# Kernel tuning notes

Hardware: AMD Instinct MI355X
Metric: run time of the kernel (lower is better)

Reference implementation:

```python
import jax, jax.numpy as jnp
import numpy as np

O, NI, F, D, NN, M = 2048, 16, 4, 128, 8, 8  # outfits, item slots, factors, dim, neighbors, valid slots
D2 = D // 2

def lrelu(x):
    return jax.nn.leaky_relu(x, 0.01)

def mlp2(x, W1, b1, W2, b2):
    # Linear -> LeakyReLU -> Linear -> LeakyReLU (Dropout is identity at inference)
    return lrelu(lrelu(x @ W1 + b1) @ W2 + b2)

def setup_inputs():
    ks = jax.random.split(jax.random.key(0), 16)
    s = 0.05
    pos = jnp.arange(NI)[None, :]
    outfit_items = jnp.where(pos < M, jax.random.randint(ks[0], (O, NI), 0, NI), -1)
    items_neighbor = jax.random.randint(ks[1], (O, NI, NN), -1, NI)
    items_feature = jax.random.normal(ks[2], (O, NI, D), dtype=jnp.float32)
    items_factors = jnp.zeros((O, NI, F, D), dtype=jnp.float32)
    p = {
        'cf_W1': jax.random.normal(ks[3], (F, D, D2)) * s,
        'cf_b1': jnp.zeros((F, D2)),
        'cf_W2': jax.random.normal(ks[4], (F, D2, D)) * s,
        'cf_b2': jnp.zeros((F, D)),
        'f2f_W1': jax.random.normal(ks[5], (D, D)) * s, 'f2f_b1': jnp.zeros((D,)),
        'f2f_W2': jax.random.normal(ks[6], (D, D)) * s, 'f2f_b2': jnp.zeros((D,)),
        'f2i_W1': jax.random.normal(ks[7], (D, D)) * s, 'f2i_b1': jnp.zeros((D,)),
        'f2i_W2': jax.random.normal(ks[8], (D, D)) * s, 'f2i_b2': jnp.zeros((D,)),
        'i2i_W1': jax.random.normal(ks[9], (D, D)) * s, 'i2i_b1': jnp.zeros((D,)),
        'i2i_W2': jax.random.normal(ks[10], (D, D)) * s, 'i2i_b2': jnp.zeros((D,)),
        'o2s_W': jax.random.normal(ks[11], (D, 1)) * s, 'o2s_b': jnp.zeros((1,)),
    }
    return dict(outfit_items=outfit_items, items_feature=items_feature,
                items_neighbor=items_neighbor, items_factors=items_factors, **p)

def _forward(outfit_items, items_feature, items_neighbor, items_factors,
             cf_W1, cf_b1, cf_W2, cf_b2, f2f_W1, f2f_b1, f2f_W2, f2f_b2,
             f2i_W1, f2i_b1, f2i_W2, f2i_b2, i2i_W1, i2i_b1, i2i_W2, i2i_b2,
             o2s_W, o2s_b):
    del items_factors  # creat_factors overwrites every entry in the original
    # --- creat_factors: per-factor 2-layer MLP on every item feature -> [O,NI,F,D]
    h = lrelu(jnp.einsum('oid,fde->oife', items_feature, cf_W1) + cf_b1)
    fac = lrelu(jnp.einsum('oife,fed->oifd', h, cf_W2) + cf_b2)

    # --- inter_factors: sequential over outfit slots; later slots read updated factors
    def outfit_fac(fac_o, oi_o, nbr_o):
        def step(f, i):
            valid = i != -1
            ic = jnp.maximum(i, 0)
            cand = jnp.concatenate([oi_o, nbr_o[ic]])                # [NI+NN]
            cm = (cand != -1) & (cand != i) & valid
            t = f[ic]                                                # [F,D] snapshot
            msg = mlp2(t[None] * f[jnp.maximum(cand, 0)],
                       f2f_W1, f2f_b1, f2f_W2, f2f_b2)               # [NI+NN,F,D]
            add = jnp.sum(jnp.where(cm[:, None, None], msg, 0.0), axis=0)
            return f.at[ic].add(jnp.where(valid, add, 0.0)), None
        f, _ = jax.lax.scan(step, fac_o, oi_o)
        return f
    fac = jax.vmap(outfit_fac)(fac, outfit_items, items_neighbor)

    # --- infer_items: feature[i] += sum_j f2i(fac[i,j]) for outfit members
    g = mlp2(fac, f2i_W1, f2i_b1, f2i_W2, f2i_b2).sum(axis=2)        # [O,NI,D]
    ic = jnp.maximum(outfit_items, 0)
    w = (outfit_items != -1).astype(g.dtype)                          # [O,NI]
    gsel = jnp.take_along_axis(g, ic[..., None], axis=1)
    scat = jax.vmap(lambda gs, idx, ww: jnp.zeros((NI, D), gs.dtype).at[idx].add(ww[:, None] * gs))
    feat = items_feature + scat(gsel, ic, w)

    # --- inter_items: sequential; current value detached (.data in original)
    def outfit_feat(fo_init, oi_o):
        jc = jnp.maximum(oi_o, 0)
        def step(fo, i):
            valid = i != -1
            ic_ = jnp.maximum(i, 0)
            t = jax.lax.stop_gradient(fo[ic_])
            msgs = mlp2(fo[jc], i2i_W1, i2i_b1, i2i_W2, i2i_b2)      # [NI,D]
            m = ((oi_o != -1) & (oi_o != i)).astype(fo.dtype)
            new = t + jnp.sum(m[:, None] * msgs, axis=0)
            return jnp.where(valid, fo.at[ic_].set(new), fo), None
        fo, _ = jax.lax.scan(step, fo_init, oi_o)
        return fo
    feat = jax.vmap(outfit_feat)(feat, outfit_items)

    # --- infer_outfit + score
    fsel = jnp.take_along_axis(feat, ic[..., None], axis=1)
    outfits = jnp.sum(w[..., None] * fsel, axis=1)                    # [O,D]
    scores = jax.nn.sigmoid(outfits @ o2s_W + o2s_b)[:, 0]            # [O]

    # --- com_loss: ||F F^T - I||_F^2 over valid slots (positional mask), / n_outfits
    G = jnp.einsum('oifd,oigd->oifg', fac, fac) - jnp.eye(F, dtype=fac.dtype)
    com = jnp.sum(w * jnp.sum(G * G, axis=(-1, -2))) / O
    return scores, jnp.reshape(com, (1,))

def reference(outfit_items, items_feature, items_neighbor, items_factors,
              cf_W1, cf_b1, cf_W2, cf_b2, f2f_W1, f2f_b1, f2f_W2, f2f_b2,
              f2i_W1, f2i_b1, f2i_W2, f2i_b2, i2i_W1, i2i_b1, i2i_W2, i2i_b2,
              o2s_W, o2s_b):
    return _forward(outfit_items, items_feature, items_neighbor, items_factors,
                    cf_W1, cf_b1, cf_W2, cf_b2, f2f_W1, f2f_b1, f2f_W2, f2f_b2,
                    f2i_W1, f2i_b1, f2i_W2, f2i_b2, i2i_W1, i2i_b1, i2i_W2, i2i_b2,
                    o2s_W, o2s_b)
```

## Files before the change

### kernel.cpp

```cpp
#include <hip/hip_runtime.h>
#include <hip/hip_bf16.h>
#include <math.h>


typedef __attribute__((ext_vector_type(8))) short short8;
typedef __attribute__((ext_vector_type(4))) float f32x4;

#define MFMA16(a, b, c) __builtin_amdgcn_mfma_f32_16x16x32_bf16(a, b, c, 0, 0, 0)

__device__ __forceinline__ float lrelu(float x) { return x > 0.0f ? x : 0.01f * x; }

__device__ __forceinline__ ushort f2bf(float f) {
  unsigned u = __builtin_bit_cast(unsigned, f);
  u += 0x7fffu + ((u >> 16) & 1u);
  return (ushort)(u >> 16);
}

__device__ __forceinline__ unsigned pk2(float a, float b) {
  float2 t; t.x = a; t.y = b;
  __hip_bfloat162 h = __float22bfloat162_rn(t);
  unsigned u;
  __builtin_memcpy(&u, &h, 4);
  return u;
}

__device__ __forceinline__ short8 load_bfrag(const float* __restrict__ W, int ldn,
                                             int kbase, int col) {
  short8 r;
#pragma unroll
  for (int j = 0; j < 8; ++j) r[j] = (short)f2bf(W[(kbase + j) * ldn + col]);
  return r;
}

__global__ void zero_com(float* out) { if (threadIdx.x == 0) out[2048] = 0.0f; }

__global__ __launch_bounds__(512, 4) void mfgn_kernel(
    const int* __restrict__ outfit_items,
    const float* __restrict__ items_feature,
    const int* __restrict__ items_neighbor,
    const float* __restrict__ cfW1, const float* __restrict__ cfb1,
    const float* __restrict__ cfW2, const float* __restrict__ cfb2,
    const float* __restrict__ f2fW1, const float* __restrict__ f2fb1,
    const float* __restrict__ f2fW2, const float* __restrict__ f2fb2,
    const float* __restrict__ f2iW1, const float* __restrict__ f2ib1,
    const float* __restrict__ f2iW2, const float* __restrict__ f2ib2,
    const float* __restrict__ i2iW1, const float* __restrict__ i2ib1,
    const float* __restrict__ i2iW2, const float* __restrict__ i2ib2,
    const float* __restrict__ o2sW, const float* __restrict__ o2sb,
    float* __restrict__ out)
{
  __shared__ float facL[16 * 528];
  __shared__ float featL[16 * 132];
  __shared__ ushort Xa[64 * 136] __attribute__((aligned(16)));
  __shared__ ushort hidB[64 * 136] __attribute__((aligned(16)));
  __shared__ float redE[8];
  __shared__ int oiL[16];
  __shared__ int nbrL[128];
  __shared__ int clAll[16 * 16];
  __shared__ int ncAll[16];
  __shared__ int vslL[16];
  __shared__ int refcntL[16];
  __shared__ int nvsL;

  const int o = blockIdx.x;
  const int tid = (int)threadIdx.x;
  const int lane = tid & 63;
  const int wid = tid >> 6;
  const int n16 = lane & 15;
  const int q = lane >> 4;
  const int kb = q * 8;
  const int col = wid * 16 + n16;

  if (tid < 16) oiL[tid] = outfit_items[o * 16 + tid];
  if (tid < 128) nbrL[tid] = items_neighbor[o * 128 + tid];
  {
    const int n = tid >> 5, d0 = (tid & 31) * 4;
    float4 v = *(const float4*)(items_feature + o * 2048 + tid * 4);
    *(float4*)(featL + n * 132 + d0) = v;
    uint2 pk; pk.x = pk2(v.x, v.y); pk.y = pk2(v.z, v.w);
    *(uint2*)(Xa + n * 136 + d0) = pk;
  }
  if (tid == 0) {
    int cnt = 0;
    for (int s = 0; s < 16; ++s) refcntL[s] = 0;
    for (int s = 0; s < 16; ++s) {
      int v = oiL[s];
      if (v != -1) { vslL[cnt++] = s; refcntL[v]++; }
    }
    nvsL = cnt;
  }
  for (int s = wid; s < 16; s += 8) {
    const int iv = outfit_items[o * 16 + s];
    if (iv == -1) { if (lane == 0) ncAll[s] = 0; continue; }
    int cand = -1;
    if (lane < 24) cand = (lane < 16) ? outfit_items[o * 16 + lane]
                                      : items_neighbor[o * 128 + iv * 8 + (lane - 16)];
    bool ok = (lane < 24) && (cand != -1) && (cand != iv);
    unsigned long long bm = __ballot(ok);
    if (ok) clAll[s * 16 + __popcll(bm & ((1ull << lane) - 1ull))] = cand;
    if (lane == 0) ncAll[s] = (int)__popcll(bm);
  }
  __syncthreads();
  const int nvs = nvsL;

  {
    const int f = wid & 3, half = wid >> 2;
    short8 wA[2][4];
#pragma unroll
    for (int etl = 0; etl < 2; ++etl)
#pragma unroll
      for (int kt = 0; kt < 4; ++kt)
        wA[etl][kt] = load_bfrag(cfW1 + f * 8192, 64, kt * 32 + kb, (half * 2 + etl) * 16 + n16);
    f32x4 acc[2];
    acc[0] = (f32x4){0.f,0.f,0.f,0.f}; acc[1] = (f32x4){0.f,0.f,0.f,0.f};
    for (int kt = 0; kt < 4; ++kt) {
      short8 x = *(const short8*)(Xa + n16 * 136 + kt * 32 + kb);
      acc[0] = MFMA16(wA[0][kt], x, acc[0]);
      acc[1] = MFMA16(wA[1][kt], x, acc[1]);
    }
#pragma unroll
    for (int etl = 0; etl < 2; ++etl) {
      f32x4 b1q = *(const f32x4*)(cfb1 + f * 64 + (half * 2 + etl) * 16 + q * 4);
      float h0 = lrelu(acc[etl][0] + b1q[0]), h1 = lrelu(acc[etl][1] + b1q[1]);
      float h2 = lrelu(acc[etl][2] + b1q[2]), h3 = lrelu(acc[etl][3] + b1q[3]);
      uint2 pk; pk.x = pk2(h0, h1); pk.y = pk2(h2, h3);
      *(uint2*)(hidB + (f * 16 + n16) * 136 + (half * 2 + etl) * 16 + q * 4) = pk;
    }
    __syncthreads();
    short8 wB[4][2];
#pragma unroll
    for (int ctl = 0; ctl < 4; ++ctl)
#pragma unroll
      for (int kt = 0; kt < 2; ++kt)
        wB[ctl][kt] = load_bfrag(cfW2 + f * 8192, 128, kt * 32 + kb, half * 64 + ctl * 16 + n16);
    f32x4 acc2[4];
#pragma unroll
    for (int ctl = 0; ctl < 4; ++ctl) acc2[ctl] = (f32x4){0.f,0.f,0.f,0.f};
    for (int kt = 0; kt < 2; ++kt) {
      short8 h = *(const short8*)(hidB + (f * 16 + n16) * 136 + kt * 32 + kb);
#pragma unroll
      for (int ctl = 0; ctl < 4; ++ctl) acc2[ctl] = MFMA16(h, wB[ctl][kt], acc2[ctl]);
    }
#pragma unroll
    for (int ctl = 0; ctl < 4; ++ctl) {
      int c = half * 64 + ctl * 16 + n16;
      float b2 = cfb2[f * 128 + c];
#pragma unroll
      for (int r = 0; r < 4; ++r)
        facL[(q * 4 + r) * 528 + f * 132 + c] = lrelu(acc2[ctl][r] + b2);
    }
    __syncthreads();
  }

  {
    short8 w1f[4], w2f[4];
#pragma unroll
    for (int kt = 0; kt < 4; ++kt) {
      w1f[kt] = load_bfrag(f2fW1, 128, kt * 32 + kb, col);
      w2f[kt] = load_bfrag(f2fW2, 128, kt * 32 + kb, col);
    }
    const f32x4 b1q = *(const f32x4*)(f2fb1 + wid * 16 + q * 4);
    const float b2v = f2fb2[col];
    const int rS = tid >> 3, kcS = tid & 7;
    const int fS = rS & 3, ciS = rS >> 2;
    const int k0 = kcS * 16;

    for (int s = 0; s < 16; ++s) {
      const int iv = oiL[s];
      if (iv == -1) continue;
      const int nc = ncAll[s];
      if (ciS < nc) {
        const int cit = clAll[s * 16 + ciS];
        const float* tp = facL + iv * 528 + fS * 132;
        const float* cp = facL + cit * 528 + fS * 132;
#pragma unroll
        for (int i2 = 0; i2 < 2; ++i2) {
          const int k = k0 + i2 * 8;
          float4 a0 = *(const float4*)(tp + k), a1 = *(const float4*)(tp + k + 4);
          float4 c0 = *(const float4*)(cp + k), c1 = *(const float4*)(cp + k + 4);
          uint4 u;
          u.x = pk2(a0.x * c0.x, a0.y * c0.y); u.y = pk2(a0.z * c0.z, a0.w * c0.w);
          u.z = pk2(a1.x * c1.x, a1.y * c1.y); u.w = pk2(a1.z * c1.z, a1.w * c1.w);
          *(uint4*)(Xa + rS * 136 + k) = u;
        }
      } else {
        uint4 z; z.x = z.y = z.z = z.w = 0;
        *(uint4*)(Xa + rS * 136 + k0) = z;
        *(uint4*)(Xa + rS * 136 + k0 + 8) = z;
      }
      __syncthreads();
      f32x4 acc[4];
#pragma unroll
      for (int mt = 0; mt < 4; ++mt) acc[mt] = (f32x4){0.f,0.f,0.f,0.f};
      for (int kt = 0; kt < 4; ++kt)
#pragma unroll
        for (int mt = 0; mt < 4; ++mt) {
          short8 x = *(const short8*)(Xa + (mt * 16 + n16) * 136 + kt * 32 + kb);
          acc[mt] = MFMA16(w1f[kt], x, acc[mt]);
        }
      __syncthreads();
#pragma unroll
      for (int mt = 0; mt < 4; ++mt) {
        float h0 = lrelu(acc[mt][0] + b1q[0]), h1 = lrelu(acc[mt][1] + b1q[1]);
        float h2 = lrelu(acc[mt][2] + b1q[2]), h3 = lrelu(acc[mt][3] + b1q[3]);
        uint2 pk; pk.x = pk2(h0, h1); pk.y = pk2(h2, h3);
        *(uint2*)(hidB + (mt * 16 + n16) * 136 + wid * 16 + q * 4) = pk;
      }
      __syncthreads();
      f32x4 acc2[4];
#pragma unroll
      for (int mt = 0; mt < 4; ++mt) acc2[mt] = (f32x4){0.f,0.f,0.f,0.f};
      for (int kt = 0; kt < 4; ++kt)
#pragma unroll
        for (int mt = 0; mt < 4; ++mt) {
          short8 h = *(const short8*)(hidB + (mt * 16 + n16) * 136 + kt * 32 + kb);
          acc2[mt] = MFMA16(h, w2f[kt], acc2[mt]);
        }
      float part[4] = {0.f, 0.f, 0.f, 0.f};
#pragma unroll
      for (int mt = 0; mt < 4; ++mt) {
        bool act = (mt * 4 + q) < nc;
        if (act)
#pragma unroll
          for (int r = 0; r < 4; ++r) part[r] += lrelu(acc2[mt][r] + b2v);
      }
#pragma unroll
      for (int r = 0; r < 4; ++r) {
        float v = part[r];
        v += __shfl_xor(v, 16);
        v += __shfl_xor(v, 32);
        part[r] = v;
      }
      if (q == 0) {
#pragma unroll
        for (int r = 0; r < 4; ++r)
          facL[iv * 528 + r * 132 + col] += part[r];
      }
      __syncthreads();
    }
  }

  {
    short8 w1f[4], w2f[4];
#pragma unroll
    for (int kt = 0; kt < 4; ++kt) {
      w1f[kt] = load_bfrag(f2iW1, 128, kt * 32 + kb, col);
      w2f[kt] = load_bfrag(f2iW2, 128, kt * 32 + kb, col);
    }
    const f32x4 b1q = *(const f32x4*)(f2ib1 + wid * 16 + q * 4);
    const float b2v = f2ib2[col];
    {
      const int r = tid >> 3, kc = tid & 7, k0 = kc * 16;
      const int f = r & 3, item = r >> 2;
      const float* sp = facL + item * 528 + f * 132;
#pragma unroll
      for (int i2 = 0; i2 < 2; ++i2) {
        const int k = k0 + i2 * 8;
        float4 a0 = *(const float4*)(sp + k), a1 = *(const float4*)(sp + k + 4);
        uint4 u;
        u.x = pk2(a0.x, a0.y); u.y = pk2(a0.z, a0.w);
        u.z = pk2(a1.x, a1.y); u.w = pk2(a1.z, a1.w);
        *(uint4*)(Xa + r * 136 + k) = u;
      }
    }
    __syncthreads();
    f32x4 acc[4];
#pragma unroll
    for (int mt = 0; mt < 4; ++mt) acc[mt] = (f32x4){0.f,0.f,0.f,0.f};
    for (int kt = 0; kt < 4; ++kt)
#pragma unroll
      for (int mt = 0; mt < 4; ++mt) {
        short8 x = *(const short8*)(Xa + (mt * 16 + n16) * 136 + kt * 32 + kb);
        acc[mt] = MFMA16(w1f[kt], x, acc[mt]);
      }
    __syncthreads();
#pragma unroll
    for (int mt = 0; mt < 4; ++mt) {
      float h0 = lrelu(acc[mt][0] + b1q[0]), h1 = lrelu(acc[mt][1] + b1q[1]);
      float h2 = lrelu(acc[mt][2] + b1q[2]), h3 = lrelu(acc[mt][3] + b1q[3]);
      uint2 pk; pk.x = pk2(h0, h1); pk.y = pk2(h2, h3);
      *(uint2*)(hidB + (mt * 16 + n16) * 136 + wid * 16 + q * 4) = pk;
    }
    __syncthreads();
    f32x4 acc2[4];
#pragma unroll
    for (int mt = 0; mt < 4; ++mt) acc2[mt] = (f32x4){0.f,0.f,0.f,0.f};
    for (int kt = 0; kt < 4; ++kt)
#pragma unroll
      for (int mt = 0; mt < 4; ++mt) {
        short8 h = *(const short8*)(hidB + (mt * 16 + n16) * 136 + kt * 32 + kb);
        acc2[mt] = MFMA16(h, w2f[kt], acc2[mt]);
      }
#pragma unroll
    for (int mt = 0; mt < 4; ++mt) {
      int item = mt * 4 + q;
      float g = 0.f;
#pragma unroll
      for (int r = 0; r < 4; ++r) g += lrelu(acc2[mt][r] + b2v);
      featL[item * 132 + col] += (float)refcntL[item] * g;
    }
    __syncthreads();
  }

  {
    short8 w1f[4], w2f[4];
#pragma unroll
    for (int kt = 0; kt < 4; ++kt) {
      w1f[kt] = load_bfrag(i2iW1, 128, kt * 32 + kb, col);
      w2f[kt] = load_bfrag(i2iW2, 128, kt * 32 + kb, col);
    }
    const f32x4 b1q = *(const f32x4*)(i2ib1 + wid * 16 + q * 4);
    const float b2v = i2ib2[col];
    const int rS = tid >> 3, kcS = tid & 7, k0 = kcS * 16;

    for (int u = 0; u < nvs; ++u) {
      const int iv = oiL[vslL[u]];
      if (rS < nvs) {
        const int it = oiL[vslL[rS]];
        const float* sp = featL + it * 132;
#pragma unroll
        for (int i2 = 0; i2 < 2; ++i2) {
          const int k = k0 + i2 * 8;
          float4 a0 = *(const float4*)(sp + k), a1 = *(const float4*)(sp + k + 4);
          uint4 uu;
          uu.x = pk2(a0.x, a0.y); uu.y = pk2(a0.z, a0.w);
          uu.z = pk2(a1.x, a1.y); uu.w = pk2(a1.z, a1.w);
          *(uint4*)(Xa + rS * 136 + k) = uu;
        }
      }
      __syncthreads();
      f32x4 acc;
      acc = (f32x4){0.f,0.f,0.f,0.f};
      for (int kt = 0; kt < 4; ++kt) {
        short8 x = *(const short8*)(Xa + n16 * 136 + kt * 32 + kb);
        acc = MFMA16(w1f[kt], x, acc);
      }
      __syncthreads();
      {
        float h0 = lrelu(acc[0] + b1q[0]), h1 = lrelu(acc[1] + b1q[1]);
        float h2 = lrelu(acc[2] + b1q[2]), h3 = lrelu(acc[3] + b1q[3]);
        uint2 pk; pk.x = pk2(h0, h1); pk.y = pk2(h2, h3);
        *(uint2*)(hidB + n16 * 136 + wid * 16 + q * 4) = pk;
      }
      __syncthreads();
      f32x4 acc2;
      acc2 = (f32x4){0.f,0.f,0.f,0.f};
      for (int kt = 0; kt < 4; ++kt) {
        short8 h = *(const short8*)(hidB + n16 * 136 + kt * 32 + kb);
        acc2 = MFMA16(h, w2f[kt], acc2);
      }
      float part = 0.f;
      if (q < 2) {
#pragma unroll
        for (int r = 0; r < 4; ++r) {
          int j = q * 4 + r;
          bool m = (j < nvs) && (oiL[vslL[j]] != iv);
          if (m) part += lrelu(acc2[r] + b2v);
        }
      }
      part += __shfl_xor(part, 16);
      if (q == 0) featL[iv * 132 + col] += part;
      __syncthreads();
    }
  }

  if (tid < 128) {
    float sum = 0.0f;
    for (int u = 0; u < nvs; ++u) sum += featL[oiL[vslL[u]] * 132 + tid];
    float v = sum * o2sW[tid];
#pragma unroll
    for (int off = 1; off < 64; off <<= 1) v += __shfl_xor(v, off);
    if (lane == 0) redE[wid] = v;
  }
  __syncthreads();
  if (tid == 0) {
    float t = redE[0] + redE[1] + o2sb[0];
    out[o] = 1.0f / (1.0f + expf(-t));
  }

  {
    const int n = tid >> 5, f = (tid >> 3) & 3, g = (tid >> 1) & 3, h = tid & 1;
    const float* pa = facL + n * 528 + f * 132 + h * 64;
    const float* pb = facL + n * 528 + g * 132 + h * 64;
    float dot = 0.0f;
    for (int i = 0; i < 16; ++i) {
      float4 a = *(const float4*)(pa + i * 4);
      float4 b = *(const float4*)(pb + i * 4);
      dot += a.x * b.x + a.y * b.y + a.z * b.z + a.w * b.w;
    }
    dot += __shfl_xor(dot, 1);
    float v = dot - ((f == g) ? 1.0f : 0.0f);
    float sq = (h == 0 && oiL[n] != -1) ? v * v : 0.0f;
#pragma unroll
    for (int off = 1; off < 64; off <<= 1) sq += __shfl_xor(sq, off);
    __syncthreads();
    if (lane == 0) redE[wid] = sq;
    __syncthreads();
    if (tid == 0) {
      float tot = 0.f;
#pragma unroll
      for (int w = 0; w < 8; ++w) tot += redE[w];
      atomicAdd(out + 2048, tot * (1.0f / 2048.0f));
    }
  }
}

extern "C" void kernel_launch(void* const* d_in, const int* in_sizes, int n_in,
                              void* d_out, int out_size, void* d_ws, size_t ws_size,
                              hipStream_t stream) {
  float* out = (float*)d_out;
  hipLaunchKernelGGL(zero_com, dim3(1), dim3(64), 0, stream, out);
  hipLaunchKernelGGL(mfgn_kernel, dim3(2048), dim3(512), 0, stream,
                     (const int*)d_in[0],
                     (const float*)d_in[1],
                     (const int*)d_in[2],
                     (const float*)d_in[4], (const float*)d_in[5],
                     (const float*)d_in[6], (const float*)d_in[7],
                     (const float*)d_in[8], (const float*)d_in[9],
                     (const float*)d_in[10], (const float*)d_in[11],
                     (const float*)d_in[12], (const float*)d_in[13],
                     (const float*)d_in[14], (const float*)d_in[15],
                     (const float*)d_in[16], (const float*)d_in[17],
                     (const float*)d_in[18], (const float*)d_in[19],
                     (const float*)d_in[20], (const float*)d_in[21],
                     out);
}
```

Before: 363.6 us.

## Store factors and features in bf16 shared memory and skip empty MFMA tiles

Factor and feature buffers in LDS change from fp32 to bf16 and are fed straight to the MFMAs, which removes the per-stage repacking copies and their barriers. An fp32 copy of each factor is kept in registers for exact accumulation, and the Gram matrix for the orthogonality loss is computed from those registers with shuffle reductions and shared atomics. The f2f MFMA loops skip row tiles beyond the candidate count. The smaller LDS footprint allows raising launch bounds to six blocks per CU. In exchange, the stored activations lose precision because feature accumulation goes through bf16 round-trips, and the i2i stage now weights neighbors by reference count over all rows.

Measured after the change: 988.9 us. 2.72x slower.

```diff
diff --git a/kernel.cpp b/kernel.cpp
--- a/kernel.cpp
+++ b/kernel.cpp
@@ -15,7 +15,12 @@
   u += 0x7fffu + ((u >> 16) & 1u);
   return (ushort)(u >> 16);
 }
-
+__device__ __forceinline__ float bflo(unsigned u) {
+  return __builtin_bit_cast(float, u << 16);
+}
+__device__ __forceinline__ float bfhi(unsigned u) {
+  return __builtin_bit_cast(float, u & 0xffff0000u);
+}
 __device__ __forceinline__ unsigned pk2(float a, float b) {
   float2 t; t.x = a; t.y = b;
   __hip_bfloat162 h = __float22bfloat162_rn(t);
@@ -23,7 +28,6 @@
   __builtin_memcpy(&u, &h, 4);
   return u;
 }
-
 __device__ __forceinline__ short8 load_bfrag(const float* __restrict__ W, int ldn,
                                              int kbase, int col) {
   short8 r;
@@ -34,7 +38,7 @@
 
 __global__ void zero_com(float* out) { if (threadIdx.x == 0) out[2048] = 0.0f; }
 
-__global__ __launch_bounds__(512, 4) void mfgn_kernel(
+__global__ __launch_bounds__(512, 6) void mfgn_kernel(
     const int* __restrict__ outfit_items,
     const float* __restrict__ items_feature,
     const int* __restrict__ items_neighbor,
@@ -49,14 +53,13 @@
     const float* __restrict__ o2sW, const float* __restrict__ o2sb,
     float* __restrict__ out)
 {
-  __shared__ float facL[16 * 528];
-  __shared__ float featL[16 * 132];
-  __shared__ ushort Xa[64 * 136] __attribute__((aligned(16)));
-  __shared__ ushort hidB[64 * 136] __attribute__((aligned(16)));
+  __shared__ ushort facB[64 * 136] __attribute__((aligned(16)));
+  __shared__ ushort featB[16 * 136] __attribute__((aligned(16)));
+  __shared__ ushort stg[64 * 136] __attribute__((aligned(16)));
+  __shared__ float comG[256];
   __shared__ float redE[8];
   __shared__ int oiL[16];
-  __shared__ int nbrL[128];
-  __shared__ int clAll[16 * 16];
+  __shared__ int clAll[256];
   __shared__ int ncAll[16];
   __shared__ int vslL[16];
   __shared__ int refcntL[16];
@@ -72,13 +75,12 @@
   const int col = wid * 16 + n16;
 
   if (tid < 16) oiL[tid] = outfit_items[o * 16 + tid];
-  if (tid < 128) nbrL[tid] = items_neighbor[o * 128 + tid];
+  if (tid < 256) comG[tid] = 0.0f;
   {
     const int n = tid >> 5, d0 = (tid & 31) * 4;
     float4 v = *(const float4*)(items_feature + o * 2048 + tid * 4);
-    *(float4*)(featL + n * 132 + d0) = v;
     uint2 pk; pk.x = pk2(v.x, v.y); pk.y = pk2(v.z, v.w);
-    *(uint2*)(Xa + n * 136 + d0) = pk;
+    *(uint2*)(featB + n * 136 + d0) = pk;
   }
   if (tid == 0) {
     int cnt = 0;
@@ -114,7 +116,7 @@
     f32x4 acc[2];
     acc[0] = (f32x4){0.f,0.f,0.f,0.f}; acc[1] = (f32x4){0.f,0.f,0.f,0.f};
     for (int kt = 0; kt < 4; ++kt) {
-      short8 x = *(const short8*)(Xa + n16 * 136 + kt * 32 + kb);
+      short8 x = *(const short8*)(featB + n16 * 136 + kt * 32 + kb);
       acc[0] = MFMA16(wA[0][kt], x, acc[0]);
       acc[1] = MFMA16(wA[1][kt], x, acc[1]);
     }
@@ -124,7 +126,7 @@
       float h0 = lrelu(acc[etl][0] + b1q[0]), h1 = lrelu(acc[etl][1] + b1q[1]);
       float h2 = lrelu(acc[etl][2] + b1q[2]), h3 = lrelu(acc[etl][3] + b1q[3]);
       uint2 pk; pk.x = pk2(h0, h1); pk.y = pk2(h2, h3);
-      *(uint2*)(hidB + (f * 16 + n16) * 136 + (half * 2 + etl) * 16 + q * 4) = pk;
+      *(uint2*)(stg + (f * 16 + n16) * 136 + (half * 2 + etl) * 16 + q * 4) = pk;
     }
     __syncthreads();
     short8 wB[4][2];
@@ -137,7 +139,7 @@
 #pragma unroll
     for (int ctl = 0; ctl < 4; ++ctl) acc2[ctl] = (f32x4){0.f,0.f,0.f,0.f};
     for (int kt = 0; kt < 2; ++kt) {
-      short8 h = *(const short8*)(hidB + (f * 16 + n16) * 136 + kt * 32 + kb);
+      short8 h = *(const short8*)(stg + (f * 16 + n16) * 136 + kt * 32 + kb);
 #pragma unroll
       for (int ctl = 0; ctl < 4; ++ctl) acc2[ctl] = MFMA16(h, wB[ctl][kt], acc2[ctl]);
     }
@@ -147,7 +149,7 @@
       float b2 = cfb2[f * 128 + c];
 #pragma unroll
       for (int r = 0; r < 4; ++r)
-        facL[(q * 4 + r) * 528 + f * 132 + c] = lrelu(acc2[ctl][r] + b2);
+        facB[((q * 4 + r) * 4 + f) * 136 + c] = f2bf(lrelu(acc2[ctl][r] + b2));
     }
     __syncthreads();
   }
@@ -161,32 +163,43 @@
     }
     const f32x4 b1q = *(const f32x4*)(f2fb1 + wid * 16 + q * 4);
     const float b2v = f2fb2[col];
+    float fac32[16];
+#pragma unroll
+    for (int rr = 0; rr < 4; ++rr)
+#pragma unroll
+      for (int f = 0; f < 4; ++f)
+        fac32[rr * 4 + f] = bflo((unsigned)facB[((q * 4 + rr) * 4 + f) * 136 + col]);
+
     const int rS = tid >> 3, kcS = tid & 7;
     const int fS = rS & 3, ciS = rS >> 2;
-    const int k0 = kcS * 16;
+    const int kcol = kcS * 16;
 
     for (int s = 0; s < 16; ++s) {
       const int iv = oiL[s];
       if (iv == -1) continue;
       const int nc = ncAll[s];
+      const int mtn = (nc + 3) >> 2;
       if (ciS < nc) {
         const int cit = clAll[s * 16 + ciS];
-        const float* tp = facL + iv * 528 + fS * 132;
-        const float* cp = facL + cit * 528 + fS * 132;
-#pragma unroll
-        for (int i2 = 0; i2 < 2; ++i2) {
-          const int k = k0 + i2 * 8;
-          float4 a0 = *(const float4*)(tp + k), a1 = *(const float4*)(tp + k + 4);
-          float4 c0 = *(const float4*)(cp + k), c1 = *(const float4*)(cp + k + 4);
-          uint4 u;
-          u.x = pk2(a0.x * c0.x, a0.y * c0.y); u.y = pk2(a0.z * c0.z, a0.w * c0.w);
-          u.z = pk2(a1.x * c1.x, a1.y * c1.y); u.w = pk2(a1.z * c1.z, a1.w * c1.w);
-          *(uint4*)(Xa + rS * 136 + k) = u;
-        }
+        const ushort* tp = facB + (iv * 4 + fS) * 136 + kcol;
+        const ushort* cp = facB + (cit * 4 + fS) * 136 + kcol;
+        uint4 ta = *(const uint4*)tp, tb = *(const uint4*)(tp + 8);
+        uint4 ca = *(const uint4*)cp, cb = *(const uint4*)(cp + 8);
+        uint4 u0, u1;
+        u0.x = pk2(bflo(ta.x) * bflo(ca.x), bfhi(ta.x) * bfhi(ca.x));
+        u0.y = pk2(bflo(ta.y) * bflo(ca.y), bfhi(ta.y) * bfhi(ca.y));
+        u0.z = pk2(bflo(ta.z) * bflo(ca.z), bfhi(ta.z) * bfhi(ca.z));
+        u0.w = pk2(bflo(ta.w) * bflo(ca.w), bfhi(ta.w) * bfhi(ca.w));
+        u1.x = pk2(bflo(tb.x) * bflo(cb.x), bfhi(tb.x) * bfhi(cb.x));
+        u1.y = pk2(bflo(tb.y) * bflo(cb.y), bfhi(tb.y) * bfhi(cb.y));
+        u1.z = pk2(bflo(tb.z) * bflo(cb.z), bfhi(tb.z) * bfhi(cb.z));
+        u1.w = pk2(bflo(tb.w) * bflo(cb.w), bfhi(tb.w) * bfhi(cb.w));
+        *(uint4*)(stg + rS * 136 + kcol) = u0;
+        *(uint4*)(stg + rS * 136 + kcol + 8) = u1;
       } else {
         uint4 z; z.x = z.y = z.z = z.w = 0;
-        *(uint4*)(Xa + rS * 136 + k0) = z;
-        *(uint4*)(Xa + rS * 136 + k0 + 8) = z;
+        *(uint4*)(stg + rS * 136 + kcol) = z;
+        *(uint4*)(stg + rS * 136 + kcol + 8) = z;
       }
       __syncthreads();
       f32x4 acc[4];
@@ -194,28 +207,31 @@
       for (int mt = 0; mt < 4; ++mt) acc[mt] = (f32x4){0.f,0.f,0.f,0.f};
       for (int kt = 0; kt < 4; ++kt)
 #pragma unroll
-        for (int mt = 0; mt < 4; ++mt) {
-          short8 x = *(const short8*)(Xa + (mt * 16 + n16) * 136 + kt * 32 + kb);
-          acc[mt] = MFMA16(w1f[kt], x, acc[mt]);
+        for (int mt = 0; mt < 4; ++mt)
+          if (mt < mtn) {
+            short8 x = *(const short8*)(stg + (mt * 16 + n16) * 136 + kt * 32 + kb);
+            acc[mt] = MFMA16(w1f[kt], x, acc[mt]);
+          }
+      __syncthreads();
+#pragma unroll
+      for (int mt = 0; mt < 4; ++mt)
+        if (mt < mtn) {
+          float h0 = lrelu(acc[mt][0] + b1q[0]), h1 = lrelu(acc[mt][1] + b1q[1]);
+          float h2 = lrelu(acc[mt][2] + b1q[2]), h3 = lrelu(acc[mt][3] + b1q[3]);
+          uint2 pk; pk.x = pk2(h0, h1); pk.y = pk2(h2, h3);
+          *(uint2*)(stg + (mt * 16 + n16) * 136 + wid * 16 + q * 4) = pk;
         }
-      __syncthreads();
-#pragma unroll
-      for (int mt = 0; mt < 4; ++mt) {
-        float h0 = lrelu(acc[mt][0] + b1q[0]), h1 = lrelu(acc[mt][1] + b1q[1]);
-        float h2 = lrelu(acc[mt][2] + b1q[2]), h3 = lrelu(acc[mt][3] + b1q[3]);
-        uint2 pk; pk.x = pk2(h0, h1); pk.y = pk2(h2, h3);
-        *(uint2*)(hidB + (mt * 16 + n16) * 136 + wid * 16 + q * 4) = pk;
-      }
       __syncthreads();
       f32x4 acc2[4];
 #pragma unroll
       for (int mt = 0; mt < 4; ++mt) acc2[mt] = (f32x4){0.f,0.f,0.f,0.f};
       for (int kt = 0; kt < 4; ++kt)
 #pragma unroll
-        for (int mt = 0; mt < 4; ++mt) {
-          short8 h = *(const short8*)(hidB + (mt * 16 + n16) * 136 + kt * 32 + kb);
-          acc2[mt] = MFMA16(h, w2f[kt], acc2[mt]);
-        }
+        for (int mt = 0; mt < 4; ++mt)
+          if (mt < mtn) {
+            short8 h = *(const short8*)(stg + (mt * 16 + n16) * 136 + kt * 32 + kb);
+            acc2[mt] = MFMA16(h, w2f[kt], acc2[mt]);
+          }
       float part[4] = {0.f, 0.f, 0.f, 0.f};
 #pragma unroll
       for (int mt = 0; mt < 4; ++mt) {
@@ -231,13 +247,30 @@
         v += __shfl_xor(v, 32);
         part[r] = v;
       }
-      if (q == 0) {
-#pragma unroll
-        for (int r = 0; r < 4; ++r)
-          facL[iv * 528 + r * 132 + col] += part[r];
-      }
-      __syncthreads();
-    }
+      if (q == (iv >> 2)) {
+        const int rr = iv & 3;
+#pragma unroll
+        for (int f = 0; f < 4; ++f) {
+          fac32[rr * 4 + f] += part[f];
+          facB[(iv * 4 + f) * 136 + col] = f2bf(fac32[rr * 4 + f]);
+        }
+      }
+      __syncthreads();
+    }
+
+#pragma unroll
+    for (int rr = 0; rr < 4; ++rr)
+#pragma unroll
+      for (int f = 0; f < 4; ++f)
+#pragma unroll
+        for (int g = 0; g < 4; ++g) {
+          float p = fac32[rr * 4 + f] * fac32[rr * 4 + g];
+          p += __shfl_xor(p, 1);
+          p += __shfl_xor(p, 2);
+          p += __shfl_xor(p, 4);
+          p += __shfl_xor(p, 8);
+          if (n16 == 0) atomicAdd(&comG[(q * 4 + rr) * 16 + f * 4 + g], p);
+        }
   }
 
   {
@@ -249,37 +282,21 @@
     }
     const f32x4 b1q = *(const f32x4*)(f2ib1 + wid * 16 + q * 4);
     const float b2v = f2ib2[col];
-    {
-      const int r = tid >> 3, kc = tid & 7, k0 = kc * 16;
-      const int f = r & 3, item = r >> 2;
-      const float* sp = facL + item * 528 + f * 132;
-#pragma unroll
-      for (int i2 = 0; i2 < 2; ++i2) {
-        const int k = k0 + i2 * 8;
-        float4 a0 = *(const float4*)(sp + k), a1 = *(const float4*)(sp + k + 4);
-        uint4 u;
-        u.x = pk2(a0.x, a0.y); u.y = pk2(a0.z, a0.w);
-        u.z = pk2(a1.x, a1.y); u.w = pk2(a1.z, a1.w);
-        *(uint4*)(Xa + r * 136 + k) = u;
-      }
-    }
-    __syncthreads();
     f32x4 acc[4];
 #pragma unroll
     for (int mt = 0; mt < 4; ++mt) acc[mt] = (f32x4){0.f,0.f,0.f,0.f};
     for (int kt = 0; kt < 4; ++kt)
 #pragma unroll
       for (int mt = 0; mt < 4; ++mt) {
-        short8 x = *(const short8*)(Xa + (mt * 16 + n16) * 136 + kt * 32 + kb);
+        short8 x = *(const short8*)(facB + (mt * 16 + n16) * 136 + kt * 32 + kb);
         acc[mt] = MFMA16(w1f[kt], x, acc[mt]);
       }
-    __syncthreads();
 #pragma unroll
     for (int mt = 0; mt < 4; ++mt) {
       float h0 = lrelu(acc[mt][0] + b1q[0]), h1 = lrelu(acc[mt][1] + b1q[1]);
       float h2 = lrelu(acc[mt][2] + b1q[2]), h3 = lrelu(acc[mt][3] + b1q[3]);
       uint2 pk; pk.x = pk2(h0, h1); pk.y = pk2(h2, h3);
-      *(uint2*)(hidB + (mt * 16 + n16) * 136 + wid * 16 + q * 4) = pk;
+      *(uint2*)(stg + (mt * 16 + n16) * 136 + wid * 16 + q * 4) = pk;
     }
     __syncthreads();
     f32x4 acc2[4];
@@ -288,7 +305,7 @@
     for (int kt = 0; kt < 4; ++kt)
 #pragma unroll
       for (int mt = 0; mt < 4; ++mt) {
-        short8 h = *(const short8*)(hidB + (mt * 16 + n16) * 136 + kt * 32 + kb);
+        short8 h = *(const short8*)(stg + (mt * 16 + n16) * 136 + kt * 32 + kb);
         acc2[mt] = MFMA16(h, w2f[kt], acc2[mt]);
       }
 #pragma unroll
@@ -297,7 +314,8 @@
       float g = 0.f;
 #pragma unroll
       for (int r = 0; r < 4; ++r) g += lrelu(acc2[mt][r] + b2v);
-      featL[item * 132 + col] += (float)refcntL[item] * g;
+      int a = item * 136 + col;
+      featB[a] = f2bf(bflo((unsigned)featB[a]) + (float)refcntL[item] * g);
     }
     __syncthreads();
   }
@@ -311,62 +329,47 @@
     }
     const f32x4 b1q = *(const f32x4*)(i2ib1 + wid * 16 + q * 4);
     const float b2v = i2ib2[col];
-    const int rS = tid >> 3, kcS = tid & 7, k0 = kcS * 16;
 
     for (int u = 0; u < nvs; ++u) {
       const int iv = oiL[vslL[u]];
-      if (rS < nvs) {
-        const int it = oiL[vslL[rS]];
-        const float* sp = featL + it * 132;
-#pragma unroll
-        for (int i2 = 0; i2 < 2; ++i2) {
-          const int k = k0 + i2 * 8;
-          float4 a0 = *(const float4*)(sp + k), a1 = *(const float4*)(sp + k + 4);
-          uint4 uu;
-          uu.x = pk2(a0.x, a0.y); uu.y = pk2(a0.z, a0.w);
-          uu.z = pk2(a1.x, a1.y); uu.w = pk2(a1.z, a1.w);
-          *(uint4*)(Xa + rS * 136 + k) = uu;
-        }
-      }
-      __syncthreads();
-      f32x4 acc;
-      acc = (f32x4){0.f,0.f,0.f,0.f};
+      f32x4 acc = (f32x4){0.f,0.f,0.f,0.f};
       for (int kt = 0; kt < 4; ++kt) {
-        short8 x = *(const short8*)(Xa + n16 * 136 + kt * 32 + kb);
+        short8 x = *(const short8*)(featB + n16 * 136 + kt * 32 + kb);
         acc = MFMA16(w1f[kt], x, acc);
       }
-      __syncthreads();
       {
         float h0 = lrelu(acc[0] + b1q[0]), h1 = lrelu(acc[1] + b1q[1]);
         float h2 = lrelu(acc[2] + b1q[2]), h3 = lrelu(acc[3] + b1q[3]);
         uint2 pk; pk.x = pk2(h0, h1); pk.y = pk2(h2, h3);
-        *(uint2*)(hidB + n16 * 136 + wid * 16 + q * 4) = pk;
-      }
-      __syncthreads();
-      f32x4 acc2;
-      acc2 = (f32x4){0.f,0.f,0.f,0.f};
+        *(uint2*)(stg + n16 * 136 + wid * 16 + q * 4) = pk;
+      }
+      __syncthreads();
+      f32x4 acc2 = (f32x4){0.f,0.f,0.f,0.f};
       for (int kt = 0; kt < 4; ++kt) {
-        short8 h = *(const short8*)(hidB + n16 * 136 + kt * 32 + kb);
+        short8 h = *(const short8*)(stg + n16 * 136 + kt * 32 + kb);
         acc2 = MFMA16(h, w2f[kt], acc2);
       }
       float part = 0.f;
-      if (q < 2) {
-#pragma unroll
-        for (int r = 0; r < 4; ++r) {
-          int j = q * 4 + r;
-          bool m = (j < nvs) && (oiL[vslL[j]] != iv);
-          if (m) part += lrelu(acc2[r] + b2v);
-        }
+#pragma unroll
+      for (int r = 0; r < 4; ++r) {
+        int item = q * 4 + r;
+        float w = (item == iv) ? 0.0f : (float)refcntL[item];
+        part += w * lrelu(acc2[r] + b2v);
       }
       part += __shfl_xor(part, 16);
-      if (q == 0) featL[iv * 132 + col] += part;
+      part += __shfl_xor(part, 32);
+      if (q == 0) {
+        int a = iv * 136 + col;
+        featB[a] = f2bf(bflo((unsigned)featB[a]) + part);
+      }
       __syncthreads();
     }
   }
 
   if (tid < 128) {
     float sum = 0.0f;
-    for (int u = 0; u < nvs; ++u) sum += featL[oiL[vslL[u]] * 132 + tid];
+    for (int u = 0; u < nvs; ++u)
+      sum += bflo((unsigned)featB[oiL[vslL[u]] * 136 + tid]);
     float v = sum * o2sW[tid];
 #pragma unroll
     for (int off = 1; off < 64; off <<= 1) v += __shfl_xor(v, off);
@@ -378,28 +381,20 @@
     out[o] = 1.0f / (1.0f + expf(-t));
   }
 
-  {
-    const int n = tid >> 5, f = (tid >> 3) & 3, g = (tid >> 1) & 3, h = tid & 1;
-    const float* pa = facL + n * 528 + f * 132 + h * 64;
-    const float* pb = facL + n * 528 + g * 132 + h * 64;
-    float dot = 0.0f;
-    for (int i = 0; i < 16; ++i) {
-      float4 a = *(const float4*)(pa + i * 4);
-      float4 b = *(const float4*)(pb + i * 4);
-      dot += a.x * b.x + a.y * b.y + a.z * b.z + a.w * b.w;
-    }
-    dot += __shfl_xor(dot, 1);
-    float v = dot - ((f == g) ? 1.0f : 0.0f);
-    float sq = (h == 0 && oiL[n] != -1) ? v * v : 0.0f;
-#pragma unroll
-    for (int off = 1; off < 64; off <<= 1) sq += __shfl_xor(sq, off);
-    __syncthreads();
-    if (lane == 0) redE[wid] = sq;
+  __syncthreads();
+  {
+    float sq = 0.0f;
+    if (tid < 256) {
+      int n = tid >> 4, f = (tid >> 2) & 3, g = tid & 3;
+      float v = comG[tid] - ((f == g) ? 1.0f : 0.0f);
+      sq = (oiL[n] != -1) ? v * v : 0.0f;
+#pragma unroll
+      for (int off = 1; off < 64; off <<= 1) sq += __shfl_xor(sq, off);
+      if (lane == 0) redE[wid] = sq;
+    }
     __syncthreads();
     if (tid == 0) {
-      float tot = 0.f;
-#pragma unroll
-      for (int w = 0; w < 8; ++w) tot += redE[w];
+      float tot = redE[0] + redE[1] + redE[2] + redE[3];
       atomicAdd(out + 2048, tot * (1.0f / 2048.0f));
     }
   }
```

## Keep item features in bf16 LDS and skip empty tiles in factor MLP

Applied to the files above, without the earlier changes.

Replaces the fp32 feature buffer with a bf16 copy that the MFMA reads directly in the item-to-item stage. This removes the per-iteration repack step and two barriers, and switches to refcount-weighted rows indexed by item. The factor-to-factor loop now skips MFMA tiles beyond the valid candidate count, and one barrier is dropped by merging the hidden-layer write into the first pass. Accumulating features in bf16 adds rounding error, and the restructured masking could change numerics or correctness.

New measurement: 464.7 us. 1.28x slower.

```diff
diff --git a/kernel.cpp b/kernel.cpp
--- a/kernel.cpp
+++ b/kernel.cpp
@@ -15,7 +15,9 @@
   u += 0x7fffu + ((u >> 16) & 1u);
   return (ushort)(u >> 16);
 }
-
+__device__ __forceinline__ float bflo(unsigned u) {
+  return __builtin_bit_cast(float, u << 16);
+}
 __device__ __forceinline__ unsigned pk2(float a, float b) {
   float2 t; t.x = a; t.y = b;
   __hip_bfloat162 h = __float22bfloat162_rn(t);
@@ -23,7 +25,6 @@
   __builtin_memcpy(&u, &h, 4);
   return u;
 }
-
 __device__ __forceinline__ short8 load_bfrag(const float* __restrict__ W, int ldn,
                                              int kbase, int col) {
   short8 r;
@@ -50,13 +51,12 @@
     float* __restrict__ out)
 {
   __shared__ float facL[16 * 528];
-  __shared__ float featL[16 * 132];
-  __shared__ ushort Xa[64 * 136] __attribute__((aligned(16)));
-  __shared__ ushort hidB[64 * 136] __attribute__((aligned(16)));
+  __shared__ ushort prodS[64 * 136] __attribute__((aligned(16)));
+  __shared__ ushort hidS[64 * 136] __attribute__((aligned(16)));
+  __shared__ ushort featB[16 * 136] __attribute__((aligned(16)));
   __shared__ float redE[8];
   __shared__ int oiL[16];
-  __shared__ int nbrL[128];
-  __shared__ int clAll[16 * 16];
+  __shared__ int clAll[256];
   __shared__ int ncAll[16];
   __shared__ int vslL[16];
   __shared__ int refcntL[16];
@@ -72,13 +72,11 @@
   const int col = wid * 16 + n16;
 
   if (tid < 16) oiL[tid] = outfit_items[o * 16 + tid];
-  if (tid < 128) nbrL[tid] = items_neighbor[o * 128 + tid];
   {
     const int n = tid >> 5, d0 = (tid & 31) * 4;
     float4 v = *(const float4*)(items_feature + o * 2048 + tid * 4);
-    *(float4*)(featL + n * 132 + d0) = v;
     uint2 pk; pk.x = pk2(v.x, v.y); pk.y = pk2(v.z, v.w);
-    *(uint2*)(Xa + n * 136 + d0) = pk;
+    *(uint2*)(featB + n * 136 + d0) = pk;
   }
   if (tid == 0) {
     int cnt = 0;
@@ -114,7 +112,7 @@
     f32x4 acc[2];
     acc[0] = (f32x4){0.f,0.f,0.f,0.f}; acc[1] = (f32x4){0.f,0.f,0.f,0.f};
     for (int kt = 0; kt < 4; ++kt) {
-      short8 x = *(const short8*)(Xa + n16 * 136 + kt * 32 + kb);
+      short8 x = *(const short8*)(featB + n16 * 136 + kt * 32 + kb);
       acc[0] = MFMA16(wA[0][kt], x, acc[0]);
       acc[1] = MFMA16(wA[1][kt], x, acc[1]);
     }
@@ -124,7 +122,7 @@
       float h0 = lrelu(acc[etl][0] + b1q[0]), h1 = lrelu(acc[etl][1] + b1q[1]);
       float h2 = lrelu(acc[etl][2] + b1q[2]), h3 = lrelu(acc[etl][3] + b1q[3]);
       uint2 pk; pk.x = pk2(h0, h1); pk.y = pk2(h2, h3);
-      *(uint2*)(hidB + (f * 16 + n16) * 136 + (half * 2 + etl) * 16 + q * 4) = pk;
+      *(uint2*)(hidS + (f * 16 + n16) * 136 + (half * 2 + etl) * 16 + q * 4) = pk;
     }
     __syncthreads();
     short8 wB[4][2];
@@ -137,7 +135,7 @@
 #pragma unroll
     for (int ctl = 0; ctl < 4; ++ctl) acc2[ctl] = (f32x4){0.f,0.f,0.f,0.f};
     for (int kt = 0; kt < 2; ++kt) {
-      short8 h = *(const short8*)(hidB + (f * 16 + n16) * 136 + kt * 32 + kb);
+      short8 h = *(const short8*)(hidS + (f * 16 + n16) * 136 + kt * 32 + kb);
 #pragma unroll
       for (int ctl = 0; ctl < 4; ++ctl) acc2[ctl] = MFMA16(h, wB[ctl][kt], acc2[ctl]);
     }
@@ -169,6 +167,7 @@
       const int iv = oiL[s];
       if (iv == -1) continue;
       const int nc = ncAll[s];
+      const int mtn = (nc + 3) >> 2;
       if (ciS < nc) {
         const int cit = clAll[s * 16 + ciS];
         const float* tp = facL + iv * 528 + fS * 132;
@@ -181,12 +180,12 @@
           uint4 u;
           u.x = pk2(a0.x * c0.x, a0.y * c0.y); u.y = pk2(a0.z * c0.z, a0.w * c0.w);
           u.z = pk2(a1.x * c1.x, a1.y * c1.y); u.w = pk2(a1.z * c1.z, a1.w * c1.w);
-          *(uint4*)(Xa + rS * 136 + k) = u;
+          *(uint4*)(prodS + rS * 136 + k) = u;
         }
       } else {
         uint4 z; z.x = z.y = z.z = z.w = 0;
-        *(uint4*)(Xa + rS * 136 + k0) = z;
-        *(uint4*)(Xa + rS * 136 + k0 + 8) = z;
+        *(uint4*)(prodS + rS * 136 + k0) = z;
+        *(uint4*)(prodS + rS * 136 + k0 + 8) = z;
       }
       __syncthreads();
       f32x4 acc[4];
@@ -194,28 +193,30 @@
       for (int mt = 0; mt < 4; ++mt) acc[mt] = (f32x4){0.f,0.f,0.f,0.f};
       for (int kt = 0; kt < 4; ++kt)
 #pragma unroll
-        for (int mt = 0; mt < 4; ++mt) {
-          short8 x = *(const short8*)(Xa + (mt * 16 + n16) * 136 + kt * 32 + kb);
-          acc[mt] = MFMA16(w1f[kt], x, acc[mt]);
+        for (int mt = 0; mt < 4; ++mt)
+          if (mt < mtn) {
+            short8 x = *(const short8*)(prodS + (mt * 16 + n16) * 136 + kt * 32 + kb);
+            acc[mt] = MFMA16(w1f[kt], x, acc[mt]);
+          }
+#pragma unroll
+      for (int mt = 0; mt < 4; ++mt)
+        if (mt < mtn) {
+          float h0 = lrelu(acc[mt][0] + b1q[0]), h1 = lrelu(acc[mt][1] + b1q[1]);
+          float h2 = lrelu(acc[mt][2] + b1q[2]), h3 = lrelu(acc[mt][3] + b1q[3]);
+          uint2 pk; pk.x = pk2(h0, h1); pk.y = pk2(h2, h3);
+          *(uint2*)(hidS + (mt * 16 + n16) * 136 + wid * 16 + q * 4) = pk;
         }
       __syncthreads();
-#pragma unroll
-      for (int mt = 0; mt < 4; ++mt) {
-        float h0 = lrelu(acc[mt][0] + b1q[0]), h1 = lrelu(acc[mt][1] + b1q[1]);
-        float h2 = lrelu(acc[mt][2] + b1q[2]), h3 = lrelu(acc[mt][3] + b1q[3]);
-        uint2 pk; pk.x = pk2(h0, h1); pk.y = pk2(h2, h3);
-        *(uint2*)(hidB + (mt * 16 + n16) * 136 + wid * 16 + q * 4) = pk;
-      }
-      __syncthreads();
       f32x4 acc2[4];
 #pragma unroll
       for (int mt = 0; mt < 4; ++mt) acc2[mt] = (f32x4){0.f,0.f,0.f,0.f};
       for (int kt = 0; kt < 4; ++kt)
 #pragma unroll
-        for (int mt = 0; mt < 4; ++mt) {
-          short8 h = *(const short8*)(hidB + (mt * 16 + n16) * 136 + kt * 32 + kb);
-          acc2[mt] = MFMA16(h, w2f[kt], acc2[mt]);
-        }
+        for (int mt = 0; mt < 4; ++mt)
+          if (mt < mtn) {
+            short8 h = *(const short8*)(hidS + (mt * 16 + n16) * 136 + kt * 32 + kb);
+            acc2[mt] = MFMA16(h, w2f[kt], acc2[mt]);
+          }
       float part[4] = {0.f, 0.f, 0.f, 0.f};
 #pragma unroll
       for (int mt = 0; mt < 4; ++mt) {
@@ -260,7 +261,7 @@
         uint4 u;
         u.x = pk2(a0.x, a0.y); u.y = pk2(a0.z, a0.w);
         u.z = pk2(a1.x, a1.y); u.w = pk2(a1.z, a1.w);
-        *(uint4*)(Xa + r * 136 + k) = u;
+        *(uint4*)(prodS + r * 136 + k) = u;
       }
     }
     __syncthreads();
@@ -270,16 +271,15 @@
     for (int kt = 0; kt < 4; ++kt)
 #pragma unroll
       for (int mt = 0; mt < 4; ++mt) {
-        short8 x = *(const short8*)(Xa + (mt * 16 + n16) * 136 + kt * 32 + kb);
+        short8 x = *(const short8*)(prodS + (mt * 16 + n16) * 136 + kt * 32 + kb);
         acc[mt] = MFMA16(w1f[kt], x, acc[mt]);
       }
-    __syncthreads();
 #pragma unroll
     for (int mt = 0; mt < 4; ++mt) {
       float h0 = lrelu(acc[mt][0] + b1q[0]), h1 = lrelu(acc[mt][1] + b1q[1]);
       float h2 = lrelu(acc[mt][2] + b1q[2]), h3 = lrelu(acc[mt][3] + b1q[3]);
       uint2 pk; pk.x = pk2(h0, h1); pk.y = pk2(h2, h3);
-      *(uint2*)(hidB + (mt * 16 + n16) * 136 + wid * 16 + q * 4) = pk;
+      *(uint2*)(hidS + (mt * 16 + n16) * 136 + wid * 16 + q * 4) = pk;
     }
     __syncthreads();
     f32x4 acc2[4];
@@ -288,7 +288,7 @@
     for (int kt = 0; kt < 4; ++kt)
 #pragma unroll
       for (int mt = 0; mt < 4; ++mt) {
-        short8 h = *(const short8*)(hidB + (mt * 16 + n16) * 136 + kt * 32 + kb);
+        short8 h = *(const short8*)(hidS + (mt * 16 + n16) * 136 + kt * 32 + kb);
         acc2[mt] = MFMA16(h, w2f[kt], acc2[mt]);
       }
 #pragma unroll
@@ -297,7 +297,8 @@
       float g = 0.f;
 #pragma unroll
       for (int r = 0; r < 4; ++r) g += lrelu(acc2[mt][r] + b2v);
-      featL[item * 132 + col] += (float)refcntL[item] * g;
+      int a = item * 136 + col;
+      featB[a] = f2bf(bflo((unsigned)featB[a]) + (float)refcntL[item] * g);
     }
     __syncthreads();
   }
@@ -311,62 +312,47 @@
     }
     const f32x4 b1q = *(const f32x4*)(i2ib1 + wid * 16 + q * 4);
     const float b2v = i2ib2[col];
-    const int rS = tid >> 3, kcS = tid & 7, k0 = kcS * 16;
 
     for (int u = 0; u < nvs; ++u) {
       const int iv = oiL[vslL[u]];
-      if (rS < nvs) {
-        const int it = oiL[vslL[rS]];
-        const float* sp = featL + it * 132;
-#pragma unroll
-        for (int i2 = 0; i2 < 2; ++i2) {
-          const int k = k0 + i2 * 8;
-          float4 a0 = *(const float4*)(sp + k), a1 = *(const float4*)(sp + k + 4);
-          uint4 uu;
-          uu.x = pk2(a0.x, a0.y); uu.y = pk2(a0.z, a0.w);
-          uu.z = pk2(a1.x, a1.y); uu.w = pk2(a1.z, a1.w);
-          *(uint4*)(Xa + rS * 136 + k) = uu;
-        }
-      }
-      __syncthreads();
-      f32x4 acc;
-      acc = (f32x4){0.f,0.f,0.f,0.f};
+      f32x4 acc = (f32x4){0.f,0.f,0.f,0.f};
       for (int kt = 0; kt < 4; ++kt) {
-        short8 x = *(const short8*)(Xa + n16 * 136 + kt * 32 + kb);
+        short8 x = *(const short8*)(featB + n16 * 136 + kt * 32 + kb);
         acc = MFMA16(w1f[kt], x, acc);
       }
-      __syncthreads();
       {
         float h0 = lrelu(acc[0] + b1q[0]), h1 = lrelu(acc[1] + b1q[1]);
         float h2 = lrelu(acc[2] + b1q[2]), h3 = lrelu(acc[3] + b1q[3]);
         uint2 pk; pk.x = pk2(h0, h1); pk.y = pk2(h2, h3);
-        *(uint2*)(hidB + n16 * 136 + wid * 16 + q * 4) = pk;
+        *(uint2*)(hidS + n16 * 136 + wid * 16 + q * 4) = pk;
       }
       __syncthreads();
-      f32x4 acc2;
-      acc2 = (f32x4){0.f,0.f,0.f,0.f};
+      f32x4 acc2 = (f32x4){0.f,0.f,0.f,0.f};
       for (int kt = 0; kt < 4; ++kt) {
-        short8 h = *(const short8*)(hidB + n16 * 136 + kt * 32 + kb);
+        short8 h = *(const short8*)(hidS + n16 * 136 + kt * 32 + kb);
         acc2 = MFMA16(h, w2f[kt], acc2);
       }
       float part = 0.f;
-      if (q < 2) {
-#pragma unroll
-        for (int r = 0; r < 4; ++r) {
-          int j = q * 4 + r;
-          bool m = (j < nvs) && (oiL[vslL[j]] != iv);
-          if (m) part += lrelu(acc2[r] + b2v);
-        }
+#pragma unroll
+      for (int r = 0; r < 4; ++r) {
+        int item = q * 4 + r;
+        float w = (item == iv) ? 0.0f : (float)refcntL[item];
+        part += w * lrelu(acc2[r] + b2v);
       }
       part += __shfl_xor(part, 16);
-      if (q == 0) featL[iv * 132 + col] += part;
+      part += __shfl_xor(part, 32);
+      if (q == 0) {
+        int a = iv * 136 + col;
+        featB[a] = f2bf(bflo((unsigned)featB[a]) + part);
+      }
       __syncthreads();
     }
   }
 
   if (tid < 128) {
     float sum = 0.0f;
-    for (int u = 0; u < nvs; ++u) sum += featL[oiL[vslL[u]] * 132 + tid];
+    for (int u = 0; u < nvs; ++u)
+      sum += bflo((unsigned)featB[oiL[vslL[u]] * 136 + tid]);
     float v = sum * o2sW[tid];
 #pragma unroll
     for (int off = 1; off < 64; off <<= 1) v += __shfl_xor(v, off);
```
